# Kernel tuning notes

Hardware: AMD Instinct MI355X
Metric: run time of the kernel (lower is better)

The kernel has to match this reference:

```python
import jax, jax.numpy as jnp
import numpy as np

VOXEL_DIM = (64, 64, 64)
VOXEL_SIZE = 0.04
STRIDE = 4.0  # backbone2d_stride


def setup_inputs() -> dict:
    key = jax.random.key(0)
    k1, k2 = jax.random.split(key, 2)
    bs, nv, cin, h, w = 4, 12, 384, 64, 64
    cout = 32
    vit_feats = jax.random.normal(k1, (bs, nv, cin, h, w), dtype=jnp.float32)
    w_reduce = jax.random.normal(k2, (cout, cin), dtype=jnp.float32) * 0.05
    b_reduce = jnp.zeros((cout,), dtype=jnp.float32)
    # Realistic pinhole projections: K @ [I | t], camera ~3m from grid center.
    rng = np.random.default_rng(0)
    f, cx, cy = 128.0, 128.0, 128.0
    K = np.array([[f, 0.0, cx], [0.0, f, cy], [0.0, 0.0, 1.0]])
    projs = np.zeros((bs, nv, 3, 4), dtype=np.float32)
    for v in range(nv):
        t = np.array([0.2 * rng.standard_normal(), 0.2 * rng.standard_normal(),
                      3.0 + 0.3 * rng.standard_normal()])
        E = np.concatenate([np.eye(3), t[:, None]], axis=1)  # 3x4
        projs[:, v] = (K @ E).astype(np.float32)
    return {"vit_feats": vit_feats, "w_reduce": w_reduce,
            "b_reduce": b_reduce, "projection": jnp.asarray(projs)}


def _backproject(proj, feats):
    """proj: (b,3,4), feats: (b,c,h,w) -> volume (b,c,N), valid (b,N)."""
    nx, ny, nz = VOXEL_DIM
    N = nx * ny * nz
    b, c, h, w = feats.shape
    X, Y, Z = jnp.meshgrid(jnp.arange(nx), jnp.arange(ny), jnp.arange(nz), indexing='ij')
    coords = jnp.stack([X.ravel(), Y.ravel(), Z.ravel()]).astype(feats.dtype)  # (3, N)
    origin = jnp.array([[-nx * VOXEL_SIZE / 2],
                        [-ny * VOXEL_SIZE / 2],
                        [-nz * VOXEL_SIZE / 2]], dtype=feats.dtype)
    world = coords * VOXEL_SIZE + origin                    # (3, N)
    world = jnp.concatenate([world, jnp.ones((1, N), feats.dtype)], axis=0)  # (4, N)
    cam = jnp.einsum('bij,jn->bin', proj, world)            # (b, 3, N)
    px = jnp.round(cam[:, 0] / cam[:, 2]).astype(jnp.int32)
    py = jnp.round(cam[:, 1] / cam[:, 2]).astype(jnp.int32)
    pz = cam[:, 2]
    valid = (px >= 0) & (py >= 0) & (px < w) & (py < h) & (pz > 0)  # (b, N)
    pxc = jnp.clip(px, 0, w - 1)
    pyc = jnp.clip(py, 0, h - 1)
    # per-batch gather: feats[b, :, py, px]
    gath = jax.vmap(lambda f, yy, xx: f[:, yy, xx])(feats, pyc, pxc)  # (b, c, N)
    vol = jnp.where(valid[:, None, :], gath, jnp.zeros((), feats.dtype))
    return vol, valid


def reference(vit_feats, w_reduce, b_reduce, projection):
    bs, nv, cin, h, w = vit_feats.shape
    cout = w_reduce.shape[0]
    nx, ny, nz = VOXEL_DIM
    N = nx * ny * nz
    # 1x1 conv channel reduction
    feats = jnp.einsum('bnchw,oc->bnohw', vit_feats, w_reduce) \
            + b_reduce[None, None, :, None, None]
    # divide intrinsics rows by the 2D backbone stride
    proj = projection.at[:, :, :2, :].set(projection[:, :, :2, :] / STRIDE)
    feats_v = jnp.moveaxis(feats, 1, 0)   # (nv, b, c, h, w)
    proj_v = jnp.moveaxis(proj, 1, 0)     # (nv, b, 3, 4)

    def step(carry, xs):
        vol, cnt = carry
        p, f = xs
        v, m = _backproject(p, f)
        return (vol + v, cnt + m.astype(vol.dtype)), None

    vol0 = jnp.zeros((bs, cout, N), jnp.float32)
    cnt0 = jnp.zeros((bs, N), jnp.float32)
    (vol, cnt), _ = jax.lax.scan(step, (vol0, cnt0), (proj_v, feats_v))
    # volume / valid, zeroed where never observed
    cnt_b = cnt[:, None, :]
    out = jnp.where(cnt_b > 0, vol / jnp.maximum(cnt_b, 1.0), jnp.zeros((), vol.dtype))
    return out.reshape(bs, cout, nx, ny, nz)
```

## Files before the change

### kernel.cpp

```cpp
#include <hip/hip_runtime.h>

#define NV 12
#define CIN 384
#define COUT 32
#define HW 4096
#define NVOX 262144
#define KSTEPS 12
#define KSTEP 32
#define KPAD 33
#define PIXB 128

typedef __attribute__((ext_vector_type(8))) short short8v;
typedef __attribute__((ext_vector_type(4))) short short4v;
typedef __attribute__((ext_vector_type(4))) float f32x4;

__device__ __forceinline__ short bf16b(float x) {
    union { float f; unsigned u; } c; c.f = x;
    unsigned r = (c.u + 0x7fffu + ((c.u >> 16) & 1u)) >> 16;
    return (short)r;
}

__global__ __launch_bounds__(256) void w_prep_kernel(
    const float* __restrict__ w, short* __restrict__ wfrag)
{
    const int t = blockIdx.x * 256 + threadIdx.x;
    const int sg = t >> 5, o = t & 31;
    const int s = sg >> 2, g = sg & 3;
    short8v v;
#pragma unroll
    for (int i = 0; i < 8; ++i)
        v[i] = bf16b(w[o * CIN + s * 32 + g * 8 + i]);
    *reinterpret_cast<short8v*>(wfrag + t * 8) = v;
}

__global__ __launch_bounds__(256) void mv_reduce_mfma_kernel(
    const float* __restrict__ vit, const short* __restrict__ wfrag,
    const float* __restrict__ bias, short* __restrict__ feats)
{
    __shared__ float lds[PIXB][KPAD];

    const int bid  = blockIdx.x;
    const int bv   = bid >> 5;
    const int pix0 = (bid & 31) * PIXB;

    const int tid  = threadIdx.x;
    const int wave = tid >> 6;
    const int l    = tid & 63;
    const int col  = l & 15;
    const int g    = l >> 4;

    const int kk  = tid >> 4;
    const int px4 = (tid & 15) * 4;

    const float* vbase = vit + (size_t)bv * CIN * HW + pix0;
    const short8v* wf  = reinterpret_cast<const short8v*>(wfrag);

    f32x4 acc00 = {0.f, 0.f, 0.f, 0.f};
    f32x4 acc01 = {0.f, 0.f, 0.f, 0.f};
    f32x4 acc10 = {0.f, 0.f, 0.f, 0.f};
    f32x4 acc11 = {0.f, 0.f, 0.f, 0.f};

#pragma unroll
    for (int s = 0; s < KSTEPS; ++s) {
        const float* r0base = vbase + (size_t)(s * KSTEP + kk) * HW;
        const float* r1base = vbase + (size_t)(s * KSTEP + kk + 16) * HW;
        const float4 r00 = *reinterpret_cast<const float4*>(r0base + px4);
        const float4 r01 = *reinterpret_cast<const float4*>(r0base + px4 + 64);
        const float4 r10 = *reinterpret_cast<const float4*>(r1base + px4);
        const float4 r11 = *reinterpret_cast<const float4*>(r1base + px4 + 64);

        __syncthreads();
        lds[px4 + 0][kk] = r00.x;  lds[px4 + 1][kk] = r00.y;
        lds[px4 + 2][kk] = r00.z;  lds[px4 + 3][kk] = r00.w;
        lds[px4 + 64][kk] = r01.x; lds[px4 + 65][kk] = r01.y;
        lds[px4 + 66][kk] = r01.z; lds[px4 + 67][kk] = r01.w;
        lds[px4 + 0][kk + 16] = r10.x;  lds[px4 + 1][kk + 16] = r10.y;
        lds[px4 + 2][kk + 16] = r10.z;  lds[px4 + 3][kk + 16] = r10.w;
        lds[px4 + 64][kk + 16] = r11.x; lds[px4 + 65][kk + 16] = r11.y;
        lds[px4 + 66][kk + 16] = r11.z; lds[px4 + 67][kk + 16] = r11.w;
        __syncthreads();

        const float4 f0a = *reinterpret_cast<const float4*>(&lds[wave * 32 + col][8 * g]);
        const float4 f0b = *reinterpret_cast<const float4*>(&lds[wave * 32 + col][8 * g + 4]);
        const float4 f1a = *reinterpret_cast<const float4*>(&lds[wave * 32 + 16 + col][8 * g]);
        const float4 f1b = *reinterpret_cast<const float4*>(&lds[wave * 32 + 16 + col][8 * g + 4]);

        short8v bfr0, bfr1;
        bfr0[0] = bf16b(f0a.x); bfr0[1] = bf16b(f0a.y);
        bfr0[2] = bf16b(f0a.z); bfr0[3] = bf16b(f0a.w);
        bfr0[4] = bf16b(f0b.x); bfr0[5] = bf16b(f0b.y);
        bfr0[6] = bf16b(f0b.z); bfr0[7] = bf16b(f0b.w);
        bfr1[0] = bf16b(f1a.x); bfr1[1] = bf16b(f1a.y);
        bfr1[2] = bf16b(f1a.z); bfr1[3] = bf16b(f1a.w);
        bfr1[4] = bf16b(f1b.x); bfr1[5] = bf16b(f1b.y);
        bfr1[6] = bf16b(f1b.z); bfr1[7] = bf16b(f1b.w);

        const short8v a0 = wf[(s * 4 + g) * 32 + col];
        const short8v a1 = wf[(s * 4 + g) * 32 + 16 + col];

        acc00 = __builtin_amdgcn_mfma_f32_16x16x32_bf16(a0, bfr0, acc00, 0, 0, 0);
        acc01 = __builtin_amdgcn_mfma_f32_16x16x32_bf16(a1, bfr0, acc01, 0, 0, 0);
        acc10 = __builtin_amdgcn_mfma_f32_16x16x32_bf16(a0, bfr1, acc10, 0, 0, 0);
        acc11 = __builtin_amdgcn_mfma_f32_16x16x32_bf16(a1, bfr1, acc11, 0, 0, 0);
    }

    const float4 b0 = *reinterpret_cast<const float4*>(bias + 4 * g);
    const float4 b1 = *reinterpret_cast<const float4*>(bias + 16 + 4 * g);
    short* dst0 = feats + ((size_t)bv * HW + pix0 + wave * 32 + col) * COUT;
    short* dst1 = dst0 + 16 * COUT;
    short4v o00, o01, o10, o11;
    o00[0] = bf16b(acc00[0] + b0.x); o00[1] = bf16b(acc00[1] + b0.y);
    o00[2] = bf16b(acc00[2] + b0.z); o00[3] = bf16b(acc00[3] + b0.w);
    o01[0] = bf16b(acc01[0] + b1.x); o01[1] = bf16b(acc01[1] + b1.y);
    o01[2] = bf16b(acc01[2] + b1.z); o01[3] = bf16b(acc01[3] + b1.w);
    o10[0] = bf16b(acc10[0] + b0.x); o10[1] = bf16b(acc10[1] + b0.y);
    o10[2] = bf16b(acc10[2] + b0.z); o10[3] = bf16b(acc10[3] + b0.w);
    o11[0] = bf16b(acc11[0] + b1.x); o11[1] = bf16b(acc11[1] + b1.y);
    o11[2] = bf16b(acc11[2] + b1.z); o11[3] = bf16b(acc11[3] + b1.w);
    *reinterpret_cast<short4v*>(dst0 + 4 * g) = o00;
    *reinterpret_cast<short4v*>(dst0 + 16 + 4 * g) = o01;
    *reinterpret_cast<short4v*>(dst1 + 4 * g) = o10;
    *reinterpret_cast<short4v*>(dst1 + 16 + 4 * g) = o11;
}

__global__ __launch_bounds__(256) void mv_fuse_kernel(
    const unsigned short* __restrict__ feats, const float* __restrict__ proj,
    float* __restrict__ out)
{
    __shared__ double P[NV][12];

    const int tid = threadIdx.x;
    const unsigned gid = blockIdx.x * 256u + tid;
    const int b = gid >> 18;
    const int n = gid & (NVOX - 1);

    if (tid < NV * 12) {
        const int v = tid / 12, e = tid - v * 12;
        const int r = e >> 2;
        const float s = (r < 2) ? 0.25f : 1.0f;
        P[v][e] = (double)(proj[((b * NV + v) * 3 + r) * 4 + (e & 3)] * s);
    }
    __syncthreads();

    const int k = n & 63, j = (n >> 6) & 63, i = n >> 12;
    const double wx = (double)i * 0.04 - 1.28;
    const double wy = (double)j * 0.04 - 1.28;
    const double wz = (double)k * 0.04 - 1.28;

    float acc[COUT];
#pragma unroll
    for (int o = 0; o < COUT; ++o) acc[o] = 0.0f;
    int cnt = 0;

    const unsigned short* fb = feats + (size_t)b * NV * HW * COUT;

    for (int v = 0; v < NV; ++v) {
        const double* p = P[v];
        const double cz = p[8] * wx + p[9] * wy + p[10] * wz + p[11];
        if (!(cz > 0.0)) continue;
        const double cx = p[0] * wx + p[1] * wy + p[2] * wz + p[3];
        const double cy = p[4] * wx + p[5] * wy + p[6] * wz + p[7];
        const double rcz = 1.0 / cz;
        const double u = rint(cx * rcz);
        const double t = rint(cy * rcz);
        if (u < 0.0 || u > 63.0 || t < 0.0 || t > 63.0) continue;
        const int px = (int)u, py = (int)t;

        const uint4* s4 = reinterpret_cast<const uint4*>(
            fb + ((size_t)(v * HW + py * 64 + px)) * COUT);
        ++cnt;
#pragma unroll
        for (int q = 0; q < 4; ++q) {
            const uint4 u4 = s4[q];
            acc[q * 8 + 0] += __uint_as_float(u4.x << 16);
            acc[q * 8 + 1] += __uint_as_float(u4.x & 0xffff0000u);
            acc[q * 8 + 2] += __uint_as_float(u4.y << 16);
            acc[q * 8 + 3] += __uint_as_float(u4.y & 0xffff0000u);
            acc[q * 8 + 4] += __uint_as_float(u4.z << 16);
            acc[q * 8 + 5] += __uint_as_float(u4.z & 0xffff0000u);
            acc[q * 8 + 6] += __uint_as_float(u4.w << 16);
            acc[q * 8 + 7] += __uint_as_float(u4.w & 0xffff0000u);
        }
    }

    const float sc = (cnt > 0) ? (1.0f / (float)cnt) : 0.0f;
    float* ob = out + (size_t)b * COUT * NVOX + n;
#pragma unroll
    for (int o = 0; o < COUT; ++o)
        ob[(size_t)o * NVOX] = acc[o] * sc;
}

extern "C" void kernel_launch(void* const* d_in, const int* in_sizes, int n_in,
                              void* d_out, int out_size, void* d_ws, size_t ws_size,
                              hipStream_t stream) {
    const float* vit  = (const float*)d_in[0];
    const float* w    = (const float*)d_in[1];
    const float* bias = (const float*)d_in[2];
    const float* proj = (const float*)d_in[3];
    float* out = (float*)d_out;

    short* wfrag = (short*)d_ws;
    short* feats = (short*)((char*)d_ws + 48 * 32 * 8 * 2);

    w_prep_kernel<<<6, 256, 0, stream>>>(w, wfrag);

    mv_reduce_mfma_kernel<<<1536, 256, 0, stream>>>(vit, wfrag, bias, feats);

    mv_fuse_kernel<<<4096, 256, 0, stream>>>(
        (const unsigned short*)feats, proj, out);
}
```

Before: 130.9 us.

## Split fuse kernel channels across four lanes with shuffled view offsets

The backprojection kernel now assigns four threads per voxel, each owning eight output channels and computing projections for three of the twelve views. View offsets are broadcast among the four lanes via shuffles, and invalid views are redirected to a zeroed feature row so the gather loop is branch-free. This aims to cut per-thread register pressure and divergence and raise occupancy, at the cost of more threads, shuffle traffic and redundant reads of the zero row.

```diff
diff --git a/kernel.cpp b/kernel.cpp
--- a/kernel.cpp
+++ b/kernel.cpp
@@ -9,6 +9,7 @@
 #define KSTEP 32
 #define KPAD 33
 #define PIXB 128
+#define ZROW_U4 786432
 
 typedef __attribute__((ext_vector_type(8))) short short8v;
 typedef __attribute__((ext_vector_type(4))) short short4v;
@@ -21,16 +22,22 @@
 }
 
 __global__ __launch_bounds__(256) void w_prep_kernel(
-    const float* __restrict__ w, short* __restrict__ wfrag)
+    const float* __restrict__ w, short* __restrict__ wfrag,
+    short* __restrict__ feats)
 {
     const int t = blockIdx.x * 256 + threadIdx.x;
-    const int sg = t >> 5, o = t & 31;
-    const int s = sg >> 2, g = sg & 3;
-    short8v v;
-#pragma unroll
-    for (int i = 0; i < 8; ++i)
-        v[i] = bf16b(w[o * CIN + s * 32 + g * 8 + i]);
-    *reinterpret_cast<short8v*>(wfrag + t * 8) = v;
+    if (t < 48 * 32) {
+        const int sg = t >> 5, o = t & 31;
+        const int s = sg >> 2, g = sg & 3;
+        short8v v;
+#pragma unroll
+        for (int i = 0; i < 8; ++i)
+            v[i] = bf16b(w[o * CIN + s * 32 + g * 8 + i]);
+        *reinterpret_cast<short8v*>(wfrag + t * 8) = v;
+    } else if (t >= 1536 && t < 1540) {
+        reinterpret_cast<uint4*>(feats)[ZROW_U4 + (t - 1536)] =
+            make_uint4(0u, 0u, 0u, 0u);
+    }
 }
 
 __global__ __launch_bounds__(256) void mv_reduce_mfma_kernel(
@@ -131,14 +138,17 @@
 
     const int tid = threadIdx.x;
     const unsigned gid = blockIdx.x * 256u + tid;
-    const int b = gid >> 18;
-    const int n = gid & (NVOX - 1);
+    const unsigned vox = gid >> 2;
+    const int r = tid & 3;
+    const int lane = tid & 63;
+    const int b = vox >> 18;
+    const int n = vox & (NVOX - 1);
 
     if (tid < NV * 12) {
         const int v = tid / 12, e = tid - v * 12;
-        const int r = e >> 2;
-        const float s = (r < 2) ? 0.25f : 1.0f;
-        P[v][e] = (double)(proj[((b * NV + v) * 3 + r) * 4 + (e & 3)] * s);
+        const int row = e >> 2;
+        const float s = (row < 2) ? 0.25f : 1.0f;
+        P[v][e] = (double)(proj[((b * NV + v) * 3 + row) * 4 + (e & 3)] * s);
     }
     __syncthreads();
 
@@ -147,47 +157,53 @@
     const double wy = (double)j * 0.04 - 1.28;
     const double wz = (double)k * 0.04 - 1.28;
 
-    float acc[COUT];
-#pragma unroll
-    for (int o = 0; o < COUT; ++o) acc[o] = 0.0f;
+    int off[3];
     int cnt = 0;
-
-    const unsigned short* fb = feats + (size_t)b * NV * HW * COUT;
-
-    for (int v = 0; v < NV; ++v) {
-        const double* p = P[v];
+    const int bbase = b * (NV * HW * 4);
+#pragma unroll
+    for (int s = 0; s < 3; ++s) {
+        const double* p = P[4 * s + r];
         const double cz = p[8] * wx + p[9] * wy + p[10] * wz + p[11];
-        if (!(cz > 0.0)) continue;
         const double cx = p[0] * wx + p[1] * wy + p[2] * wz + p[3];
         const double cy = p[4] * wx + p[5] * wy + p[6] * wz + p[7];
-        const double rcz = 1.0 / cz;
-        const double u = rint(cx * rcz);
-        const double t = rint(cy * rcz);
-        if (u < 0.0 || u > 63.0 || t < 0.0 || t > 63.0) continue;
-        const int px = (int)u, py = (int)t;
-
-        const uint4* s4 = reinterpret_cast<const uint4*>(
-            fb + ((size_t)(v * HW + py * 64 + px)) * COUT);
-        ++cnt;
-#pragma unroll
-        for (int q = 0; q < 4; ++q) {
-            const uint4 u4 = s4[q];
-            acc[q * 8 + 0] += __uint_as_float(u4.x << 16);
-            acc[q * 8 + 1] += __uint_as_float(u4.x & 0xffff0000u);
-            acc[q * 8 + 2] += __uint_as_float(u4.y << 16);
-            acc[q * 8 + 3] += __uint_as_float(u4.y & 0xffff0000u);
-            acc[q * 8 + 4] += __uint_as_float(u4.z << 16);
-            acc[q * 8 + 5] += __uint_as_float(u4.z & 0xffff0000u);
-            acc[q * 8 + 6] += __uint_as_float(u4.w << 16);
-            acc[q * 8 + 7] += __uint_as_float(u4.w & 0xffff0000u);
-        }
+        const double u = rint(cx / cz);
+        const double t = rint(cy / cz);
+        const bool valid = (cz > 0.0) & (u >= 0.0) & (u <= 63.0) &
+                           (t >= 0.0) & (t <= 63.0);
+        const double uc = fmin(fmax(u, 0.0), 63.0);
+        const double tc = fmin(fmax(t, 0.0), 63.0);
+        const int pix = (int)uc + 64 * (int)tc;
+        off[s] = valid ? (bbase + ((4 * s + r) * HW + pix) * 4) : ZROW_U4;
+        cnt += valid ? 1 : 0;
+    }
+    cnt += __shfl_xor(cnt, 1);
+    cnt += __shfl_xor(cnt, 2);
+
+    float acc[8];
+#pragma unroll
+    for (int q = 0; q < 8; ++q) acc[q] = 0.0f;
+
+    const uint4* f4 = reinterpret_cast<const uint4*>(feats);
+#pragma unroll
+    for (int v = 0; v < NV; ++v) {
+        const int src = (lane & ~3) | (v & 3);
+        const int ov = __shfl(off[v >> 2], src, 64);
+        const uint4 u4 = f4[ov + r];
+        acc[0] += __uint_as_float(u4.x << 16);
+        acc[1] += __uint_as_float(u4.x & 0xffff0000u);
+        acc[2] += __uint_as_float(u4.y << 16);
+        acc[3] += __uint_as_float(u4.y & 0xffff0000u);
+        acc[4] += __uint_as_float(u4.z << 16);
+        acc[5] += __uint_as_float(u4.z & 0xffff0000u);
+        acc[6] += __uint_as_float(u4.w << 16);
+        acc[7] += __uint_as_float(u4.w & 0xffff0000u);
     }
 
     const float sc = (cnt > 0) ? (1.0f / (float)cnt) : 0.0f;
-    float* ob = out + (size_t)b * COUT * NVOX + n;
-#pragma unroll
-    for (int o = 0; o < COUT; ++o)
-        ob[(size_t)o * NVOX] = acc[o] * sc;
+    float* ob = out + (size_t)b * COUT * NVOX + (size_t)(8 * r) * NVOX + n;
+#pragma unroll
+    for (int q = 0; q < 8; ++q)
+        ob[(size_t)q * NVOX] = acc[q] * sc;
 }
 
 extern "C" void kernel_launch(void* const* d_in, const int* in_sizes, int n_in,
@@ -202,10 +218,10 @@
     short* wfrag = (short*)d_ws;
     short* feats = (short*)((char*)d_ws + 48 * 32 * 8 * 2);
 
-    w_prep_kernel<<<6, 256, 0, stream>>>(w, wfrag);
+    w_prep_kernel<<<7, 256, 0, stream>>>(w, wfrag, feats);
 
     mv_reduce_mfma_kernel<<<1536, 256, 0, stream>>>(vit, wfrag, bias, feats);
 
-    mv_fuse_kernel<<<4096, 256, 0, stream>>>(
+    mv_fuse_kernel<<<16384, 256, 0, stream>>>(
         (const unsigned short*)feats, proj, out);
 }
```

Result: no change. 131.4 us (+0.4%).
